# Kernel tuning notes

Measured on AMD Instinct MI355X. Metric: run time of the kernel, lower is better.

Reference implementation:

```python
import jax, jax.numpy as jnp
import numpy as np

B, T, N, F_IN, F_OUT, E = 4, 12, 2048, 64, 64, 32768


def setup_inputs() -> dict:
    key = jax.random.key(0)
    ks = jax.random.split(key, 10)
    s = 1.0 / np.sqrt(F_IN)
    return {
        "x": jax.random.normal(ks[0], (B, T, N, F_IN), dtype=jnp.float32),
        "edge_index": jax.random.randint(ks[1], (2, E), 0, N, dtype=jnp.int64),
        "Wk": jax.random.normal(ks[2], (F_IN, F_OUT), dtype=jnp.float32) * s,
        "bk": jax.random.normal(ks[3], (F_OUT,), dtype=jnp.float32) * s,
        "Wq": jax.random.normal(ks[4], (F_IN, F_OUT), dtype=jnp.float32) * s,
        "bq": jax.random.normal(ks[5], (F_OUT,), dtype=jnp.float32) * s,
        "Wv": jax.random.normal(ks[6], (F_IN, F_OUT), dtype=jnp.float32) * s,
        "bv": jax.random.normal(ks[7], (F_OUT,), dtype=jnp.float32) * s,
        "Wskip": jax.random.normal(ks[8], (F_IN, F_OUT), dtype=jnp.float32) * s,
        "bias": jax.random.normal(ks[9], (F_OUT,), dtype=jnp.float32) * s,
    }


def reference(x, edge_index, Wk, bk, Wq, bq, Wv, bv, Wskip, bias):
    b, t, n, _ = x.shape
    xs = x.reshape(b * t, n, -1)                       # (b t) n f
    # per-node projections (small GEMMs)
    k = xs @ Wk + bk                                   # key from target nodes
    q = xs @ Wq + bq                                   # query from source nodes
    v = xs @ Wv + bv                                   # value from source nodes
    src, dst = edge_index[0], edge_index[1]            # j -> i (source_to_target)
    # per-edge gate + message: LeakyReLU(k_i + q_j) * v_j  [(b t), E, f_out]
    msg = jax.nn.leaky_relu(k[:, dst] + q[:, src], negative_slope=0.01) * v[:, src]
    # scatter-add aggregation at target nodes
    agg = jnp.zeros_like(k).at[:, dst].add(msg)
    out = agg + xs @ Wskip + bias
    return out.reshape(b, t, n, -1)
```

## Files before the change

### kernel.cpp

```cpp
#include <hip/hip_runtime.h>

#define BT 48
#define NN 2048
#define FF 64
#define EE 32768
#define ROWS (BT*NN)
#define PROJ_BLKS 768
#define CSR_BLKS 64

typedef __attribute__((ext_vector_type(2))) _Float16 half2v;
typedef __attribute__((ext_vector_type(8))) _Float16 half8v;
typedef __attribute__((ext_vector_type(4))) float float4v;

__device__ __forceinline__ unsigned cvt2h(float lo, float hi){
    union { half2v h; unsigned u; } c;
    c.h = half2v{(_Float16)lo, (_Float16)hi};
    return c.u;
}
__device__ __forceinline__ half2v h2(unsigned u){
    union { unsigned u; half2v h; } c; c.u = u; return c.h;
}

union FragH { unsigned u[4]; half8v h; uint4 u4; };

__global__ __launch_bounds__(256) void wpack_kernel(
    const float* __restrict__ Wk, const float* __restrict__ Wq,
    const float* __restrict__ Wv, const float* __restrict__ Ws,
    unsigned* __restrict__ Wp, int* __restrict__ meta)
{
    const int t = threadIdx.x;
    if (t < 8) meta[t] = 0;
    for (int idx = t; idx < 8192; idx += 256){
        const int mat = idx >> 11;
        const int r   = idx & 2047;
        const int ft  = r >> 9;
        const int h   = (r >> 8) & 1;
        const int l   = (r >> 2) & 63;
        const int jj  = r & 3;
        const float* W = (mat==0)?Wk:(mat==1)?Wq:(mat==2)?Wv:Ws;
        const int k0 = h*32 + (l>>4)*8 + 2*jj;
        const int c  = ft*16 + (l&15);
        Wp[idx] = cvt2h(W[(size_t)k0*FF + c], W[(size_t)(k0+1)*FF + c]);
    }
}

__device__ __forceinline__ void gbar(int* ctr, int nblk){
    __syncthreads();
    if (threadIdx.x == 0){
        __threadfence();
        atomicAdd(ctr, 1);
        while (__hip_atomic_load(ctr, __ATOMIC_ACQUIRE, __HIP_MEMORY_SCOPE_AGENT) < nblk) {}
    }
    __syncthreads();
}

__global__ __launch_bounds__(256) void projcsr_kernel(
    const float* __restrict__ x, const unsigned* __restrict__ Wp,
    const float* __restrict__ bk, const float* __restrict__ bq,
    const float* __restrict__ bv, const float* __restrict__ bs,
    unsigned* __restrict__ Kh, unsigned* __restrict__ QV,
    float* __restrict__ out,
    const unsigned int* __restrict__ ew,
    int* __restrict__ flag, int* __restrict__ bar,
    int* __restrict__ deg, int* __restrict__ offs,
    int* __restrict__ cur, int* __restrict__ elist)
{
    if (blockIdx.x >= PROJ_BLKS){
        const int t = threadIdx.x;
        const int gtid = (blockIdx.x - PROJ_BLKS)*256 + t;

        for (int i=gtid; i<NN; i+=16384) deg[i] = 0;
        if (gtid < 16) elist[EE + gtid] = 0;
        unsigned f = 0;
        for (int i=gtid; i<8192; i+=16384) f |= ew[2*i+1];
        if (f) atomicOr((unsigned int*)flag, f);
        gbar(bar+0, CSR_BLKS);
        const bool i64 = (*flag == 0);

        for (int e=gtid; e<EE; e+=16384){
            const int d = i64 ? (int)ew[2*(EE+e)] : (int)ew[EE+e];
            atomicAdd(&deg[d], 1);
        }
        gbar(bar+1, CSR_BLKS);

        if (blockIdx.x == PROJ_BLKS){
            __shared__ int wsums[4];
            const int base = t*8;
            int v[8], pre[8];
            #pragma unroll
            for (int j=0;j<8;j++) v[j] = deg[base+j];
            pre[0] = 0;
            #pragma unroll
            for (int j=1;j<8;j++) pre[j] = pre[j-1] + v[j-1];
            const int s = pre[7] + v[7];
            int inc = s;
            const int lane = t & 63, wid = t >> 6;
            #pragma unroll
            for (int d=1; d<64; d<<=1){ int tt = __shfl_up(inc, d, 64); if (lane>=d) inc += tt; }
            if (lane == 63) wsums[wid] = inc;
            __syncthreads();
            if (t == 0){ int a=0; for (int k2=0;k2<4;k2++){ int tt=wsums[k2]; wsums[k2]=a; a+=tt; } }
            __syncthreads();
            const int excl = wsums[wid] + (inc - s);
            #pragma unroll
            for (int j=0;j<8;j++){ offs[base+j] = excl + pre[j]; cur[base+j] = excl + pre[j]; }
            if (t == 255) offs[NN] = excl + s;
        }
        gbar(bar+2, CSR_BLKS);

        for (int e=gtid; e<EE; e+=16384){
            int d, s;
            if (i64){ d = (int)ew[2*(EE+e)]; s = (int)ew[2*e]; }
            else    { d = (int)ew[EE+e];     s = (int)ew[e];   }
            const int pos = atomicAdd(&cur[d], 1);
            elist[pos] = s;
        }
        return;
    }

    const int tid = threadIdx.x;
    const int w  = tid >> 6;
    const int l  = tid & 63;
    const int lr = l & 15;
    const int lh = l >> 4;
    const int wm = w & 1;
    const int matA = wm ? 1 : 0;
    const int matB = wm ? 2 : 3;
    const float* bmA = wm ? bq : bk;
    const float* bmB = wm ? bv : bs;

    FragH afA[4][2], afB[4][2];
    #pragma unroll
    for (int ft=0;ft<4;ft++)
        #pragma unroll
        for (int h=0;h<2;h++){
            afA[ft][h].u4 = *(const uint4*)(Wp + ((matA*4+ft)*2+h)*256 + l*4);
            afB[ft][h].u4 = *(const uint4*)(Wp + ((matB*4+ft)*2+h)*256 + l*4);
        }
    float4 biasA[4], biasB[4];
    #pragma unroll
    for (int ft=0;ft<4;ft++){
        biasA[ft] = *(const float4*)(bmA + ft*16 + lh*4);
        biasB[ft] = *(const float4*)(bmB + ft*16 + lh*4);
    }

    const int row0 = blockIdx.x * 128 + (w>>1)*64;
    #pragma unroll 2
    for (int rt=0; rt<4; ++rt){
        const int r16 = row0 + rt*16;
        const float* xr = x + (size_t)(r16 + lr)*FF + lh*8;
        const float4 xa0 = *(const float4*)(xr);
        const float4 xa1 = *(const float4*)(xr + 4);
        const float4 xb0 = *(const float4*)(xr + 32);
        const float4 xb1 = *(const float4*)(xr + 36);
        FragH b0, b1;
        b0.u[0]=cvt2h(xa0.x,xa0.y); b0.u[1]=cvt2h(xa0.z,xa0.w);
        b0.u[2]=cvt2h(xa1.x,xa1.y); b0.u[3]=cvt2h(xa1.z,xa1.w);
        b1.u[0]=cvt2h(xb0.x,xb0.y); b1.u[1]=cvt2h(xb0.z,xb0.w);
        b1.u[2]=cvt2h(xb1.x,xb1.y); b1.u[3]=cvt2h(xb1.z,xb1.w);

        const size_t row = (size_t)(r16 + lr);
        #pragma unroll
        for (int ft=0;ft<4;ft++){
            float4v aA = float4v{biasA[ft].x, biasA[ft].y, biasA[ft].z, biasA[ft].w};
            aA = __builtin_amdgcn_mfma_f32_16x16x32_f16(afA[ft][0].h, b0.h, aA, 0,0,0);
            aA = __builtin_amdgcn_mfma_f32_16x16x32_f16(afA[ft][1].h, b1.h, aA, 0,0,0);
            float4v aB = float4v{biasB[ft].x, biasB[ft].y, biasB[ft].z, biasB[ft].w};
            aB = __builtin_amdgcn_mfma_f32_16x16x32_f16(afB[ft][0].h, b0.h, aB, 0,0,0);
            aB = __builtin_amdgcn_mfma_f32_16x16x32_f16(afB[ft][1].h, b1.h, aB, 0,0,0);
            if (wm == 0){
                uint2 st; st.x = cvt2h(aA[0],aA[1]); st.y = cvt2h(aA[2],aA[3]);
                *(uint2*)(Kh + row*32 + ft*8 + lh*2) = st;
                *(float4*)(out + row*FF + ft*16 + lh*4) =
                    make_float4(aB[0],aB[1],aB[2],aB[3]);
            } else {
                uint4 st;
                st.x = cvt2h(aA[0],aA[1]); st.y = cvt2h(aB[0],aB[1]);
                st.z = cvt2h(aA[2],aA[3]); st.w = cvt2h(aB[2],aB[3]);
                *(uint4*)(QV + row*FF + ft*16 + lh*4) = st;
            }
        }
    }
}

#define HEDGE2(U, KA, KB, A01, A23) { \
    half2v g01 = (KA) + h2((U).x); \
    g01 = __builtin_elementwise_max(g01, g01*c001); \
    (A01) += g01 * h2((U).y); \
    half2v g23 = (KB) + h2((U).z); \
    g23 = __builtin_elementwise_max(g23, g23*c001); \
    (A23) += g23 * h2((U).w); }
#define HEDGE2M(U, KA, KB, A01, A23, M) { \
    half2v g01 = (KA) + h2((U).x); \
    g01 = __builtin_elementwise_max(g01, g01*c001); \
    (A01) += g01 * (h2((U).y) * (M)); \
    half2v g23 = (KB) + h2((U).z); \
    g23 = __builtin_elementwise_max(g23, g23*c001); \
    (A23) += g23 * (h2((U).w) * (M)); }

__global__ __launch_bounds__(256) void agg_kernel(
    const unsigned* __restrict__ Kh, const unsigned* __restrict__ QV,
    const int* __restrict__ offs, const int* __restrict__ elist,
    float* __restrict__ out)
{
    const int tid  = threadIdx.x;
    const int lane = tid & 63;
    const int w    = tid >> 6;
    const int b    = blockIdx.x;
    const int xcd  = b & 7;
    const int li   = b >> 3;
    const int pr   = xcd*3 + (li >> 9);
    const int node = ((li & 511) << 2) | w;
    const int sub  = lane >> 4;
    const int fq   = lane & 15;
    const int bt0  = pr*2;
    const size_t S = (size_t)NN*FF;

    const uint2 ku0 = *(const uint2*)(Kh + ((size_t)bt0*NN + node)*32 + 2*fq);
    const uint2 ku1 = *(const uint2*)(Kh + ((size_t)(bt0+1)*NN + node)*32 + 2*fq);
    const size_t r0 = ((size_t)bt0*NN + node)*FF;
    const size_t r1 = r0 + S;
    const float4 sk0 = *(const float4*)(out + r0 + fq*4);
    const float4 sk1 = *(const float4*)(out + r1 + fq*4);

    const half2v k01a = h2(ku0.x), k23a = h2(ku0.y);
    const half2v k01b = h2(ku1.x), k23b = h2(ku1.y);
    const half2v c001 = half2v{(_Float16)0.01f, (_Float16)0.01f};
    const half2v one2 = half2v{(_Float16)1.f, (_Float16)1.f};
    const half2v zero2 = half2v{(_Float16)0.f, (_Float16)0.f};
    const unsigned* QV0 = QV + (size_t)bt0*S;
    const unsigned* QV1 = QV0 + S;

    half2v a01_0 = zero2, a23_0 = zero2;
    half2v a01_1 = zero2, a23_1 = zero2;
    const int s0 = offs[node], s1 = offs[node+1];

    for (int i = s0; i < s1; i += 16){
        const int rem  = s1 - i;
        const int4 ev = *(const int4*)(elist + i + 4*sub);
        const unsigned o0 = (((unsigned)ev.x)<<6) + (fq<<2);
        const unsigned o1 = (((unsigned)ev.y)<<6) + (fq<<2);
        const unsigned o2 = (((unsigned)ev.z)<<6) + (fq<<2);
        const unsigned o3 = (((unsigned)ev.w)<<6) + (fq<<2);
        const uint4 u00 = *(const uint4*)(QV0 + o0);
        const uint4 u10 = *(const uint4*)(QV1 + o0);
        const uint4 u01 = *(const uint4*)(QV0 + o1);
        const uint4 u11 = *(const uint4*)(QV1 + o1);
        const uint4 u02 = *(const uint4*)(QV0 + o2);
        const uint4 u12 = *(const uint4*)(QV1 + o2);
        const uint4 u03 = *(const uint4*)(QV0 + o3);
        const uint4 u13 = *(const uint4*)(QV1 + o3);
        if (rem >= 16){
            HEDGE2(u00, k01a, k23a, a01_0, a23_0); HEDGE2(u10, k01b, k23b, a01_1, a23_1);
            HEDGE2(u01, k01a, k23a, a01_0, a23_0); HEDGE2(u11, k01b, k23b, a01_1, a23_1);
            HEDGE2(u02, k01a, k23a, a01_0, a23_0); HEDGE2(u12, k01b, k23b, a01_1, a23_1);
            HEDGE2(u03, k01a, k23a, a01_0, a23_0); HEDGE2(u13, k01b, k23b, a01_1, a23_1);
        } else {
            const half2v m0 = (4*sub+0 < rem) ? one2 : zero2;
            const half2v m1 = (4*sub+1 < rem) ? one2 : zero2;
            const half2v m2 = (4*sub+2 < rem) ? one2 : zero2;
            const half2v m3 = (4*sub+3 < rem) ? one2 : zero2;
            HEDGE2M(u00, k01a, k23a, a01_0, a23_0, m0); HEDGE2M(u10, k01b, k23b, a01_1, a23_1, m0);
            HEDGE2M(u01, k01a, k23a, a01_0, a23_0, m1); HEDGE2M(u11, k01b, k23b, a01_1, a23_1, m1);
            HEDGE2M(u02, k01a, k23a, a01_0, a23_0, m2); HEDGE2M(u12, k01b, k23b, a01_1, a23_1, m2);
            HEDGE2M(u03, k01a, k23a, a01_0, a23_0, m3); HEDGE2M(u13, k01b, k23b, a01_1, a23_1, m3);
        }
    }

    float4 ac0 = make_float4((float)a01_0[0], (float)a01_0[1],
                             (float)a23_0[0], (float)a23_0[1]);
    float4 ac1 = make_float4((float)a01_1[0], (float)a01_1[1],
                             (float)a23_1[0], (float)a23_1[1]);

    ac0.x += __shfl_xor(ac0.x, 16, 64); ac0.y += __shfl_xor(ac0.y, 16, 64);
    ac0.z += __shfl_xor(ac0.z, 16, 64); ac0.w += __shfl_xor(ac0.w, 16, 64);
    ac0.x += __shfl_xor(ac0.x, 32, 64); ac0.y += __shfl_xor(ac0.y, 32, 64);
    ac0.z += __shfl_xor(ac0.z, 32, 64); ac0.w += __shfl_xor(ac0.w, 32, 64);
    ac1.x += __shfl_xor(ac1.x, 16, 64); ac1.y += __shfl_xor(ac1.y, 16, 64);
    ac1.z += __shfl_xor(ac1.z, 16, 64); ac1.w += __shfl_xor(ac1.w, 16, 64);
    ac1.x += __shfl_xor(ac1.x, 32, 64); ac1.y += __shfl_xor(ac1.y, 32, 64);
    ac1.z += __shfl_xor(ac1.z, 32, 64); ac1.w += __shfl_xor(ac1.w, 32, 64);

    if (sub == 0){
        *(float4*)(out + r0 + fq*4) =
            make_float4(ac0.x+sk0.x, ac0.y+sk0.y, ac0.z+sk0.z, ac0.w+sk0.w);
        *(float4*)(out + r1 + fq*4) =
            make_float4(ac1.x+sk1.x, ac1.y+sk1.y, ac1.z+sk1.z, ac1.w+sk1.w);
    }
}

extern "C" void kernel_launch(void* const* d_in, const int* in_sizes, int n_in,
                              void* d_out, int out_size, void* d_ws, size_t ws_size,
                              hipStream_t stream)
{
    const float* x  = (const float*)d_in[0];
    const unsigned int* ew = (const unsigned int*)d_in[1];
    const float* Wk = (const float*)d_in[2];
    const float* bk = (const float*)d_in[3];
    const float* Wq = (const float*)d_in[4];
    const float* bq = (const float*)d_in[5];
    const float* Wv = (const float*)d_in[6];
    const float* bv = (const float*)d_in[7];
    const float* Ws = (const float*)d_in[8];
    const float* bs = (const float*)d_in[9];
    float* out = (float*)d_out;

    const size_t n = (size_t)ROWS*FF;
    unsigned* Kh = (unsigned*)d_ws;
    unsigned* QV = Kh + (size_t)ROWS*32;
    unsigned* Wp = QV + n;
    int* meta  = (int*)(Wp + 8192);
    int* flag  = meta;
    int* bar   = meta + 4;
    int* deg   = meta + 16;
    int* offs  = deg + NN;
    int* cur   = offs + NN + 16;
    int* elist = cur + NN;

    hipLaunchKernelGGL(wpack_kernel, dim3(1), dim3(256), 0, stream,
                       Wk, Wq, Wv, Ws, Wp, meta);
    hipLaunchKernelGGL(projcsr_kernel, dim3(PROJ_BLKS + CSR_BLKS), dim3(256), 0, stream,
                       x, Wp, bk, bq, bv, bs, Kh, QV, out,
                       ew, flag, bar, deg, offs, cur, elist);
    hipLaunchKernelGGL(agg_kernel, dim3(ROWS/8), dim3(256), 0, stream,
                       Kh, QV, offs, elist, out);
}
```

Before: 93.37 us.

## Split projection work so each wave computes one weight matrix over 64 rows

Changes the projection kernel from each wave computing two weight matrices over 64 rows (128 rows per block) to each wave computing a single matrix over the block's 64 rows. The block count doubles to cover the same rows. This halves per-wave register fragments and MFMA work, which raises occupancy and parallelism. The cost is that each block reads x four times, and Q and V are now written as interleaved scalar 32-bit stores instead of a single 128-bit store.

New measurement: 103.0 us. 1.1x slower.

```diff
diff --git a/kernel.cpp b/kernel.cpp
--- a/kernel.cpp
+++ b/kernel.cpp
@@ -5,7 +5,7 @@
 #define FF 64
 #define EE 32768
 #define ROWS (BT*NN)
-#define PROJ_BLKS 768
+#define PROJ_BLKS 1536
 #define CSR_BLKS 64
 
 typedef __attribute__((ext_vector_type(2))) _Float16 half2v;
@@ -65,6 +65,8 @@
     int* __restrict__ deg, int* __restrict__ offs,
     int* __restrict__ cur, int* __restrict__ elist)
 {
+    __shared__ int wsums[4];
+
     if (blockIdx.x >= PROJ_BLKS){
         const int t = threadIdx.x;
         const int gtid = (blockIdx.x - PROJ_BLKS)*256 + t;
@@ -84,7 +86,6 @@
         gbar(bar+1, CSR_BLKS);
 
         if (blockIdx.x == PROJ_BLKS){
-            __shared__ int wsums[4];
             const int base = t*8;
             int v[8], pre[8];
             #pragma unroll
@@ -123,28 +124,20 @@
     const int l  = tid & 63;
     const int lr = l & 15;
     const int lh = l >> 4;
-    const int wm = w & 1;
-    const int matA = wm ? 1 : 0;
-    const int matB = wm ? 2 : 3;
-    const float* bmA = wm ? bq : bk;
-    const float* bmB = wm ? bv : bs;
-
-    FragH afA[4][2], afB[4][2];
+    const float* bm = (w==0)?bk:(w==1)?bq:(w==2)?bv:bs;
+
+    FragH af[4][2];
     #pragma unroll
     for (int ft=0;ft<4;ft++)
         #pragma unroll
-        for (int h=0;h<2;h++){
-            afA[ft][h].u4 = *(const uint4*)(Wp + ((matA*4+ft)*2+h)*256 + l*4);
-            afB[ft][h].u4 = *(const uint4*)(Wp + ((matB*4+ft)*2+h)*256 + l*4);
-        }
-    float4 biasA[4], biasB[4];
+        for (int h=0;h<2;h++)
+            af[ft][h].u4 = *(const uint4*)(Wp + ((w*4+ft)*2+h)*256 + l*4);
+
+    float4 bias4[4];
     #pragma unroll
-    for (int ft=0;ft<4;ft++){
-        biasA[ft] = *(const float4*)(bmA + ft*16 + lh*4);
-        biasB[ft] = *(const float4*)(bmB + ft*16 + lh*4);
-    }
-
-    const int row0 = blockIdx.x * 128 + (w>>1)*64;
+    for (int ft=0;ft<4;ft++) bias4[ft] = *(const float4*)(bm + ft*16 + lh*4);
+
+    const int row0 = blockIdx.x * 64;
     #pragma unroll 2
     for (int rt=0; rt<4; ++rt){
         const int r16 = row0 + rt*16;
@@ -162,22 +155,22 @@
         const size_t row = (size_t)(r16 + lr);
         #pragma unroll
         for (int ft=0;ft<4;ft++){
-            float4v aA = float4v{biasA[ft].x, biasA[ft].y, biasA[ft].z, biasA[ft].w};
-            aA = __builtin_amdgcn_mfma_f32_16x16x32_f16(afA[ft][0].h, b0.h, aA, 0,0,0);
-            aA = __builtin_amdgcn_mfma_f32_16x16x32_f16(afA[ft][1].h, b1.h, aA, 0,0,0);
-            float4v aB = float4v{biasB[ft].x, biasB[ft].y, biasB[ft].z, biasB[ft].w};
-            aB = __builtin_amdgcn_mfma_f32_16x16x32_f16(afB[ft][0].h, b0.h, aB, 0,0,0);
-            aB = __builtin_amdgcn_mfma_f32_16x16x32_f16(afB[ft][1].h, b1.h, aB, 0,0,0);
-            if (wm == 0){
-                uint2 st; st.x = cvt2h(aA[0],aA[1]); st.y = cvt2h(aA[2],aA[3]);
-                *(uint2*)(Kh + row*32 + ft*8 + lh*2) = st;
+            float4v acc = float4v{bias4[ft].x, bias4[ft].y, bias4[ft].z, bias4[ft].w};
+            acc = __builtin_amdgcn_mfma_f32_16x16x32_f16(af[ft][0].h, b0.h, acc, 0,0,0);
+            acc = __builtin_amdgcn_mfma_f32_16x16x32_f16(af[ft][1].h, b1.h, acc, 0,0,0);
+            const int p0 = ft*8 + lh*2;
+            if (w == 0){
+                uint2 st; st.x = cvt2h(acc[0],acc[1]); st.y = cvt2h(acc[2],acc[3]);
+                *(uint2*)(Kh + row*32 + p0) = st;
+            } else if (w == 1){
+                QV[row*FF + 2*p0]     = cvt2h(acc[0],acc[1]);
+                QV[row*FF + 2*(p0+1)] = cvt2h(acc[2],acc[3]);
+            } else if (w == 2){
+                QV[row*FF + 2*p0 + 1]     = cvt2h(acc[0],acc[1]);
+                QV[row*FF + 2*(p0+1) + 1] = cvt2h(acc[2],acc[3]);
+            } else {
                 *(float4*)(out + row*FF + ft*16 + lh*4) =
-                    make_float4(aB[0],aB[1],aB[2],aB[3]);
-            } else {
-                uint4 st;
-                st.x = cvt2h(aA[0],aA[1]); st.y = cvt2h(aB[0],aB[1]);
-                st.z = cvt2h(aA[2],aA[3]); st.w = cvt2h(aB[2],aB[3]);
-                *(uint4*)(QV + row*FF + ft*16 + lh*4) = st;
+                    make_float4(acc[0],acc[1],acc[2],acc[3]);
             }
         }
     }
```
